# Kernel optimization log

Hardware: AMD Instinct MI355X
Metric: run time of the kernel (lower is better)

Reference implementation:

```python
import jax, jax.numpy as jnp
import numpy as np
from jax import lax

EPS = 1e-5


def setup_inputs() -> dict:
    key = jax.random.key(0)
    ks = jax.random.split(key, 4)
    B, C, H, W = 8, 256, 64, 64
    G, K = 4, 3
    x = jax.random.normal(ks[0], (B, C, H, W), dtype=jnp.float32)
    # offset/mask branch conv: 3*G*K*K output channels (2 offsets + 1 mask per point)
    w_off = jax.random.normal(ks[1], (3 * G * K * K, C, K, K), dtype=jnp.float32) * 0.01
    b_off = jnp.zeros((3 * G * K * K,), dtype=jnp.float32)
    # deformable conv weight, grouped: [C_out, C_in//G, K, K]
    w_dcn = jax.random.normal(ks[2], (C, C // G, K, K), dtype=jnp.float32) * (1.0 / np.sqrt(C // G * K * K))
    b_dcn = jnp.zeros((C,), dtype=jnp.float32)
    gamma = jnp.ones((C,), dtype=jnp.float32)
    beta = jnp.zeros((C,), dtype=jnp.float32)
    return {"x": x, "w_off": w_off, "b_off": b_off, "w_dcn": w_dcn,
            "b_dcn": b_dcn, "gamma": gamma, "beta": beta}


def _bilinear_gather(flat, idx, valid, B, G, Cg, KK, H, W):
    # flat: [B,G,Cg,H*W]; idx, valid: [B,G,KK,H,W]
    idx_f = idx.reshape(B, G, 1, KK * H * W)
    vals = jnp.take_along_axis(flat, idx_f, axis=3)  # [B,G,Cg,KK*H*W]
    vals = vals.reshape(B, G, Cg, KK, H, W)
    return vals * valid[:, :, None].astype(flat.dtype)


def _dcn_forward(x, w_off, b_off, w_dcn, b_dcn, gamma, beta):
    B, C, H, W = x.shape
    G, K = 4, 3
    KK = K * K
    Cg = C // G
    pad = K // 2
    dn = ("NCHW", "OIHW", "NCHW")

    # offset / modulation branch
    off = lax.conv_general_dilated(x, w_off, (1, 1), "SAME", dimension_numbers=dn)
    off = off + b_off[None, :, None, None]
    offsets = off[:, : 2 * G * KK].reshape(B, G, KK, 2, H, W)
    mask = jax.nn.sigmoid(off[:, 2 * G * KK:]).reshape(B, G, KK, H, W)

    # sampling locations: output pixel + kernel offset + learned offset
    ky, kx = jnp.meshgrid(jnp.arange(K) - pad, jnp.arange(K) - pad, indexing="ij")
    ky = ky.reshape(KK).astype(x.dtype)
    kx = kx.reshape(KK).astype(x.dtype)
    hh = jnp.arange(H, dtype=x.dtype)[:, None]          # [H,1]
    ww = jnp.arange(W, dtype=x.dtype)[None, :]          # [1,W]
    py = hh[None, None, None] + ky[None, None, :, None, None] + offsets[:, :, :, 0]  # [B,G,KK,H,W]
    px = ww[None, None, None] + kx[None, None, :, None, None] + offsets[:, :, :, 1]

    y0 = jnp.floor(py); x0 = jnp.floor(px)
    wy1 = py - y0; wy0 = 1.0 - wy1
    wx1 = px - x0; wx0 = 1.0 - wx1
    y0i = y0.astype(jnp.int32); x0i = x0.astype(jnp.int32)
    y1i = y0i + 1; x1i = x0i + 1

    flat = x.reshape(B, G, Cg, H * W)

    def corner(yi, xi, wgt):
        valid = (yi >= 0) & (yi < H) & (xi >= 0) & (xi < W)
        idx = jnp.clip(yi, 0, H - 1) * W + jnp.clip(xi, 0, W - 1)
        v = _bilinear_gather(flat, idx, valid, B, G, Cg, KK, H, W)
        return v * wgt[:, :, None]

    sampled = (corner(y0i, x0i, wy0 * wx0) + corner(y0i, x1i, wy0 * wx1)
               + corner(y1i, x0i, wy1 * wx0) + corner(y1i, x1i, wy1 * wx1))
    sampled = sampled * mask[:, :, None]                 # [B,G,Cg,KK,H,W]

    wg = w_dcn.reshape(G, C // G, Cg, KK)                # [G, Cout_g, Cin_g, KK]
    out = jnp.einsum("bgckhw,gock->bgohw", sampled, wg).reshape(B, C, H, W)
    out = out + b_dcn[None, :, None, None]

    # LayerNorm over channel dim (applied in BHWC layout)
    a = out.transpose(0, 2, 3, 1)                        # [B,H,W,C]
    mu = jnp.mean(a, axis=-1, keepdims=True)
    var = jnp.mean(jnp.square(a - mu), axis=-1, keepdims=True)
    normed = (a - mu) * lax.rsqrt(var + EPS) * gamma + beta
    attn = jax.nn.sigmoid(normed).transpose(0, 3, 1, 2)  # [B,C,H,W]
    return x * attn


def reference(x, w_off, b_off, w_dcn, b_dcn, gamma, beta):
    return _dcn_forward(x, w_off, b_off, w_dcn, b_dcn, gamma, beta)
```

## Files before the change

### kernel.cpp

```cpp
#include <hip/hip_runtime.h>
#include <hip/hip_bf16.h>
#include <math.h>


typedef __attribute__((ext_vector_type(4))) short s16x4;
typedef __attribute__((ext_vector_type(8))) short s16x8;
typedef __attribute__((ext_vector_type(4))) float f32x4;

union S8 { s16x8 v; s16x4 h[2]; };
union S8U { s16x8 v; unsigned u[4]; };

__device__ __forceinline__ s16x8 ld8(const short* p) {
  S8 r;
  r.h[0] = *(const s16x4*)p;
  r.h[1] = *(const s16x4*)(p + 4);
  return r.v;
}

__device__ __forceinline__ unsigned short bfr(float v) {
  unsigned u = __float_as_uint(v);
  u = (u + 0x7FFFu + ((u >> 16) & 1u)) >> 16;
  return (unsigned short)u;
}
__device__ __forceinline__ float bff(unsigned short s) {
  return __uint_as_float(((unsigned)s) << 16);
}
__device__ __forceinline__ float bf(short s) {
  return __uint_as_float(((unsigned)(unsigned short)s) << 16);
}
__device__ __forceinline__ unsigned cvtpk(float lo, float hi) {
  union { __hip_bfloat162 b; unsigned u; } cv;
  cv.b = __float22bfloat162_rn(make_float2(lo, hi));
  return cv.u;
}

__global__ __launch_bounds__(256) void k_prep(
    const float* __restrict__ w_off, const float* __restrict__ w_dcn,
    short* __restrict__ wo_a, short* __restrict__ wd_a) {
  int i = blockIdx.x * 256 + threadIdx.x;
  const int n1 = 112 * 2304;
  if (i < n1) {
    int e = i & 7;
    int t1 = i >> 3;
    int lane = t1 & 63;
    int t2 = t1 >> 6;
    int mt = t2 % 7;
    int t3 = t2 / 7;
    int s = t3 & 1;
    int t4 = t3 >> 1;
    int tap = t4 % 9;
    int part = t4 / 9;
    int co = mt * 16 + (lane & 15);
    int ch = part * 64 + s * 32 + (lane >> 4) * 8 + e;
    float v = (co < 108) ? w_off[(co * 256 + ch) * 9 + tap] : 0.f;
    wo_a[i] = (short)bfr(v);
  } else {
    int j = i - n1;
    int g = j / 36864, r = j % 36864;
    int tap = r >> 12;
    int q = r & 4095;
    int co = q >> 6, cl = q & 63;
    wd_a[j] = (short)bfr(w_dcn[((g * 64 + co) * 64 + cl) * 9 + tap]);
  }
}

__global__ __launch_bounds__(256) void k_x2(
    const float* __restrict__ x, short* __restrict__ x2) {
  int id = blockIdx.x * 256 + threadIdx.x;
  const int n1 = 8 * 32 * 4096;
  if (id < n1) {
    int pc = id & 4095;
    int c2 = (id >> 12) & 31;
    int b = id >> 17;
    int h = pc >> 6, w = pc & 63;
    const float* xp = x + ((size_t)(b * 256 + c2 * 8)) * 4096 + pc;
    short* o = x2 + ((size_t)(b * 32 + c2) * 4356 + (h + 1) * 66 + (w + 1)) * 8;
    s16x4 v0, v1;
#pragma unroll
    for (int i = 0; i < 4; ++i) {
      v0[i] = (short)bfr(xp[(size_t)i * 4096]);
      v1[i] = (short)bfr(xp[(size_t)(i + 4) * 4096]);
    }
    *(s16x4*)o = v0;
    *(s16x4*)(o + 4) = v1;
  } else {
    int j = id - n1;
    int plane = j / 260, r = j % 260;
    int h, w;
    if (r < 66) { h = 0; w = r; }
    else if (r < 132) { h = 65; w = r - 66; }
    else if (r < 196) { h = r - 131; w = 0; }
    else { h = r - 195; w = 65; }
    short* o = x2 + ((size_t)plane * 4356 + h * 66 + w) * 8;
    s16x4 z = {0, 0, 0, 0};
    *(s16x4*)o = z;
    *(s16x4*)(o + 4) = z;
  }
}

__global__ __launch_bounds__(256) void k_offconv(
    const short* __restrict__ x2, const short* __restrict__ wo_a,
    const float* __restrict__ b_off, short* __restrict__ wpart) {
  __shared__ short p_s[4 * 66 * 68];
  int bi = blockIdx.x;
  int xcd = bi & 7;
  int j = bi >> 3;
  int slice = xcd * 4 + (j & 3);
  int h0 = (j >> 2) * 2;
  int part = slice >> 3, b = slice & 7;
  int tid = threadIdx.x;
  int lane = tid & 63, wv = tid >> 6;
  int quad = lane >> 4, l15 = lane & 15;

  f32x4 zero4 = {0.f, 0.f, 0.f, 0.f};
  f32x4 acc[7][2];
#pragma unroll
  for (int i = 0; i < 7; ++i)
#pragma unroll
    for (int r = 0; r < 2; ++r) acc[i][r] = zero4;

  const short* x2b = x2 + (size_t)(b * 32 + part * 8) * 34848;
  const short* wfrag = wo_a + (size_t)part * 64512 + lane * 8;

  for (int it = tid; it < 2112; it += 256) {
    int ck = it / 264;
    int rp = it - ck * 264;
    const short* src = x2b + (size_t)ck * 34848 + ((size_t)h0 * 66 + rp) * 8;
    S8 v;
    v.v = *(const s16x8*)src;
    short* dst = &p_s[rp * 68 + ck * 8];
    *(s16x4*)dst = v.h[0];
    *(s16x4*)(dst + 4) = v.h[1];
  }
  __syncthreads();

  int nb = 16 * wv + l15;
#pragma unroll
  for (int tap = 0; tap < 9; ++tap) {
    int ky = tap / 3, kx = tap % 3;
#pragma unroll
    for (int s = 0; s < 2; ++s) {
      int k0 = 32 * s + quad * 8;
      const short* wb = wfrag + (size_t)(tap * 2 + s) * 3584;
      s16x8 af[7];
#pragma unroll
      for (int mt = 0; mt < 7; ++mt)
        af[mt] = *(const s16x8*)(wb + (size_t)mt * 512);
#pragma unroll
      for (int r = 0; r < 2; ++r) {
        s16x8 bf_f = ld8(&p_s[((r + ky) * 66 + nb + kx) * 68 + k0]);
#pragma unroll
        for (int mt = 0; mt < 7; ++mt)
          acc[mt][r] =
              __builtin_amdgcn_mfma_f32_16x16x32_bf16(af[mt], bf_f, acc[mt][r], 0, 0, 0);
      }
    }
  }

  short* wp = wpart + ((size_t)part * 8 + b) * 108 * 4096;
#pragma unroll
  for (int mt = 0; mt < 7; ++mt) {
#pragma unroll
    for (int rr = 0; rr < 2; ++rr) {
#pragma unroll
      for (int r = 0; r < 4; ++r) {
        int co = 16 * mt + quad * 4 + r;
        if (co < 108) {
          float v = acc[mt][rr][r] + (part == 0 ? b_off[co] : 0.f);
          wp[(size_t)co * 4096 + (h0 + rr) * 64 + nb] = (short)bfr(v);
        }
      }
    }
  }
}

__global__ __launch_bounds__(256) void k_dcn(
    const short* __restrict__ x2, const short* __restrict__ wpart,
    const short* __restrict__ wd_a, const float* __restrict__ b_dcn,
    float* __restrict__ dcn) {
  __shared__ float4 prm[9][64];
  __shared__ short wlds[2][64][72];

  int bi = blockIdx.x;
  int xcd = bi & 7;
  int j = bi >> 3;
  int grp = xcd * 4 + (j & 3);
  int h = j >> 2;
  int b = grp >> 2, g = grp & 3;
  int tid = threadIdx.x;
  int lane = tid & 63, wv = tid >> 6;
  int quad = lane >> 4, l15 = lane & 15;
  int px = 16 * wv + l15;

  f32x4 zero4 = {0.f, 0.f, 0.f, 0.f};
  f32x4 acc[4];
#pragma unroll
  for (int i = 0; i < 4; ++i) acc[i] = zero4;

  const short* x2g = x2 + (size_t)(b * 32 + g * 8) * 34848;
  const short* plA = x2g + (size_t)quad * 34848;
  const short* plB = x2g + (size_t)(quad + 4) * 34848;
  const short* wd_g = wd_a + (size_t)g * 36864;

  int co_w = tid >> 2, kp_w = (tid & 3) * 16;

  {
    const short* wsrc = wd_g + co_w * 64 + kp_w;
    s16x8 w0 = *(const s16x8*)wsrc;
    s16x8 w1 = *(const s16x8*)(wsrc + 8);
    *(s16x8*)&wlds[0][co_w][kp_w] = w0;
    *(s16x8*)&wlds[0][co_w][kp_w + 8] = w1;
  }
  for (int i = tid; i < 576; i += 256) {
    int c = i >> 6, pxa = i & 63;
    int sp = h * 64 + pxa;
    int co_y = (g * 9 + c) * 2;
    float oy = 0.f, ox = 0.f, mz = 0.f;
#pragma unroll
    for (int p4 = 0; p4 < 4; ++p4) {
      const short* wp = wpart + ((size_t)p4 * 8 + b) * 108 * 4096;
      oy += bff((unsigned short)wp[(size_t)co_y * 4096 + sp]);
      ox += bff((unsigned short)wp[(size_t)(co_y + 1) * 4096 + sp]);
      mz += bff((unsigned short)wp[(size_t)(72 + g * 9 + c) * 4096 + sp]);
    }
    float m = 1.f / (1.f + __expf(-mz));
    float py = (float)h + (float)(c / 3 - 1) + oy;
    float pxf = (float)pxa + (float)(c % 3 - 1) + ox;
    prm[c][pxa] = make_float4(py, pxf, m, 0.f);
  }
  __syncthreads();

  s16x8 cA[2][4], cB[2][4];
  float4 wts[2];

  auto stage = [&](int c, int st) {
    float4 pr = prm[c][px];
    float py = pr.x, pxf = pr.y, m = pr.z;
    float y0 = floorf(py), x0 = floorf(pxf);
    float wy1 = py - y0, wy0 = 1.f - wy1;
    float wx1 = pxf - x0, wx0 = 1.f - wx1;
    int y0i = (int)y0, x0i = (int)x0;
    int y1i = y0i + 1, x1i = x0i + 1;
    bool vy0 = (y0i >= 0) & (y0i < 64), vy1 = (y1i >= 0) & (y1i < 64);
    bool vx0 = (x0i >= 0) & (x0i < 64), vx1 = (x1i >= 0) & (x1i < 64);
    int cy0 = min(max(y0i, 0), 63) + 1, cy1 = min(max(y1i, 0), 63) + 1;
    int cx0 = min(max(x0i, 0), 63) + 1, cx1 = min(max(x1i, 0), 63) + 1;
    int i00 = cy0 * 66 + cx0, i01 = cy0 * 66 + cx1;
    int i10 = cy1 * 66 + cx0, i11 = cy1 * 66 + cx1;
    wts[st] = make_float4((vy0 && vx0) ? wy0 * wx0 * m : 0.f,
                          (vy0 && vx1) ? wy0 * wx1 * m : 0.f,
                          (vy1 && vx0) ? wy1 * wx0 * m : 0.f,
                          (vy1 && vx1) ? wy1 * wx1 * m : 0.f);
    cA[st][0] = *(const s16x8*)(plA + (size_t)i00 * 8);
    cA[st][1] = *(const s16x8*)(plA + (size_t)i01 * 8);
    cA[st][2] = *(const s16x8*)(plA + (size_t)i10 * 8);
    cA[st][3] = *(const s16x8*)(plA + (size_t)i11 * 8);
    cB[st][0] = *(const s16x8*)(plB + (size_t)i00 * 8);
    cB[st][1] = *(const s16x8*)(plB + (size_t)i01 * 8);
    cB[st][2] = *(const s16x8*)(plB + (size_t)i10 * 8);
    cB[st][3] = *(const s16x8*)(plB + (size_t)i11 * 8);
  };

  stage(0, 0);
#pragma unroll
  for (int c = 0; c < 9; ++c) {
    int cur = c & 1;
    s16x8 wn0, wn1;
    if (c < 8) {
      const short* wsrc = wd_g + (size_t)(c + 1) * 4096 + co_w * 64 + kp_w;
      wn0 = *(const s16x8*)wsrc;
      wn1 = *(const s16x8*)(wsrc + 8);
      stage(c + 1, cur ^ 1);
    }

    float4 w = wts[cur];
    S8U bf0, bf1;
#pragma unroll
    for (int i2 = 0; i2 < 4; ++i2) {
      int e0 = 2 * i2, e1 = 2 * i2 + 1;
      float vA0 = w.x * bf(cA[cur][0][e0]) + w.y * bf(cA[cur][1][e0]) +
                  w.z * bf(cA[cur][2][e0]) + w.w * bf(cA[cur][3][e0]);
      float vA1 = w.x * bf(cA[cur][0][e1]) + w.y * bf(cA[cur][1][e1]) +
                  w.z * bf(cA[cur][2][e1]) + w.w * bf(cA[cur][3][e1]);
      float vB0 = w.x * bf(cB[cur][0][e0]) + w.y * bf(cB[cur][1][e0]) +
                  w.z * bf(cB[cur][2][e0]) + w.w * bf(cB[cur][3][e0]);
      float vB1 = w.x * bf(cB[cur][0][e1]) + w.y * bf(cB[cur][1][e1]) +
                  w.z * bf(cB[cur][2][e1]) + w.w * bf(cB[cur][3][e1]);
      bf0.u[i2] = cvtpk(vA0, vA1);
      bf1.u[i2] = cvtpk(vB0, vB1);
    }

#pragma unroll
    for (int mt = 0; mt < 4; ++mt) {
      s16x8 af = *(const s16x8*)&wlds[cur][16 * mt + l15][quad * 8];
      acc[mt] = __builtin_amdgcn_mfma_f32_16x16x32_bf16(af, bf0.v, acc[mt], 0, 0, 0);
    }
#pragma unroll
    for (int mt = 0; mt < 4; ++mt) {
      s16x8 af = *(const s16x8*)&wlds[cur][16 * mt + l15][32 + quad * 8];
      acc[mt] = __builtin_amdgcn_mfma_f32_16x16x32_bf16(af, bf1.v, acc[mt], 0, 0, 0);
    }

    if (c < 8) {
      *(s16x8*)&wlds[cur ^ 1][co_w][kp_w] = wn0;
      *(s16x8*)&wlds[cur ^ 1][co_w][kp_w + 8] = wn1;
      __syncthreads();
    }
  }

  int nb = px;
#pragma unroll
  for (int mt = 0; mt < 4; ++mt) {
#pragma unroll
    for (int r = 0; r < 4; ++r) {
      int co = 16 * mt + quad * 4 + r;
      dcn[(((size_t)b * 256 + g * 64 + co) * 64 + h) * 64 + nb] =
          acc[mt][r] + b_dcn[g * 64 + co];
    }
  }
}

__global__ __launch_bounds__(256) void k_ln(
    const float* __restrict__ dcn, const float* __restrict__ x,
    const float* __restrict__ gamma, const float* __restrict__ beta,
    float* __restrict__ out) {
  __shared__ float red_s[4][64];
  __shared__ float red_q[4][64];
  int px = threadIdx.x & 63;
  int part = threadIdx.x >> 6;
  int p = blockIdx.x * 64 + px;
  int b = p >> 12, hw = p & 4095;
  const float* ob = dcn + (size_t)b * 256 * 4096 + hw;
  const float* xb = x + (size_t)b * 256 * 4096 + hw;
  float* yb = out + (size_t)b * 256 * 4096 + hw;
  int c0 = part * 64;
  float v[64];
  float s = 0.f, s2 = 0.f;
#pragma unroll
  for (int i = 0; i < 64; ++i) {
    v[i] = ob[(c0 + i) * 4096];
    s += v[i];
    s2 += v[i] * v[i];
  }
  red_s[part][px] = s;
  red_q[part][px] = s2;
  __syncthreads();
  s = red_s[0][px] + red_s[1][px] + red_s[2][px] + red_s[3][px];
  s2 = red_q[0][px] + red_q[1][px] + red_q[2][px] + red_q[3][px];
  float mu = s * (1.f / 256.f);
  float var = s2 * (1.f / 256.f) - mu * mu;
  float rs = rsqrtf(var + 1e-5f);
#pragma unroll
  for (int i = 0; i < 64; ++i) {
    int c = c0 + i;
    float nrm = (v[i] - mu) * rs * gamma[c] + beta[c];
    float attn = 1.f / (1.f + __expf(-nrm));
    yb[c * 4096] = xb[c * 4096] * attn;
  }
}

extern "C" void kernel_launch(void* const* d_in, const int* in_sizes, int n_in,
                              void* d_out, int out_size, void* d_ws,
                              size_t ws_size, hipStream_t stream) {
  const float* x = (const float*)d_in[0];
  const float* w_off = (const float*)d_in[1];
  const float* b_off = (const float*)d_in[2];
  const float* w_dcn = (const float*)d_in[3];
  const float* b_dcn = (const float*)d_in[4];
  const float* gamma = (const float*)d_in[5];
  const float* beta = (const float*)d_in[6];
  float* out = (float*)d_out;
  char* wsb = (char*)d_ws;

  short* wpart = (short*)wsb;
  short* wo_a = (short*)(wsb + 28311552);
  short* wd_a = (short*)(wsb + 28827648);
  short* x2 = (short*)(wsb + 29122560);
  float* dcnb = out;

  k_prep<<<1584, 256, 0, stream>>>(w_off, w_dcn, wo_a, wd_a);
  k_x2<<<4356, 256, 0, stream>>>(x, x2);
  k_offconv<<<1024, 256, 0, stream>>>(x2, wo_a, b_off, wpart);
  k_dcn<<<2048, 256, 0, stream>>>(x2, wpart, wd_a, b_dcn, dcnb);
  k_ln<<<512, 256, 0, stream>>>(dcnb, x, gamma, beta, out);
}
```

Baseline: 193.1 us.

## Repartition offset-conv MFMA tiles across waves by output-channel instead of pixel

In the offset conv kernel, each wave now owns one or two 16-channel output tiles (waves 0-2 get two, wave 3 gets one) across all 64 pixels. Previously every wave held all seven channel tiles for its own 16-pixel strip. Each wave now loads at most two weight fragments per step from global memory instead of seven, and reads four LDS B-fragments per row instead of one. This cuts redundant weight traffic and accumulator registers, but leaves the last wave with half the MFMA work, so the load across waves is uneven.

```diff
diff --git a/kernel.cpp b/kernel.cpp
--- a/kernel.cpp
+++ b/kernel.cpp
@@ -112,12 +112,17 @@
   int lane = tid & 63, wv = tid >> 6;
   int quad = lane >> 4, l15 = lane & 15;
 
+  int mt0 = 2 * wv;
+  bool two = (wv < 3);
+
   f32x4 zero4 = {0.f, 0.f, 0.f, 0.f};
-  f32x4 acc[7][2];
-#pragma unroll
-  for (int i = 0; i < 7; ++i)
-#pragma unroll
-    for (int r = 0; r < 2; ++r) acc[i][r] = zero4;
+  f32x4 acc[2][2][4];
+#pragma unroll
+  for (int a = 0; a < 2; ++a)
+#pragma unroll
+    for (int r = 0; r < 2; ++r)
+#pragma unroll
+      for (int p = 0; p < 4; ++p) acc[a][r][p] = zero4;
 
   const short* x2b = x2 + (size_t)(b * 32 + part * 8) * 34848;
   const short* wfrag = wo_a + (size_t)part * 64512 + lane * 8;
@@ -134,7 +139,6 @@
   }
   __syncthreads();
 
-  int nb = 16 * wv + l15;
 #pragma unroll
   for (int tap = 0; tap < 9; ++tap) {
     int ky = tap / 3, kx = tap % 3;
@@ -142,32 +146,41 @@
     for (int s = 0; s < 2; ++s) {
       int k0 = 32 * s + quad * 8;
       const short* wb = wfrag + (size_t)(tap * 2 + s) * 3584;
-      s16x8 af[7];
-#pragma unroll
-      for (int mt = 0; mt < 7; ++mt)
-        af[mt] = *(const s16x8*)(wb + (size_t)mt * 512);
-#pragma unroll
-      for (int r = 0; r < 2; ++r) {
-        s16x8 bf_f = ld8(&p_s[((r + ky) * 66 + nb + kx) * 68 + k0]);
-#pragma unroll
-        for (int mt = 0; mt < 7; ++mt)
-          acc[mt][r] =
-              __builtin_amdgcn_mfma_f32_16x16x32_bf16(af[mt], bf_f, acc[mt][r], 0, 0, 0);
+      s16x8 af0 = *(const s16x8*)(wb + (size_t)mt0 * 512);
+      s16x8 af1 = af0;
+      if (two) af1 = *(const s16x8*)(wb + (size_t)(mt0 + 1) * 512);
+#pragma unroll
+      for (int rr = 0; rr < 2; ++rr) {
+#pragma unroll
+        for (int pg = 0; pg < 4; ++pg) {
+          s16x8 bf_f = ld8(&p_s[((rr + ky) * 66 + pg * 16 + l15 + kx) * 68 + k0]);
+          acc[0][rr][pg] =
+              __builtin_amdgcn_mfma_f32_16x16x32_bf16(af0, bf_f, acc[0][rr][pg], 0, 0, 0);
+          if (two)
+            acc[1][rr][pg] =
+                __builtin_amdgcn_mfma_f32_16x16x32_bf16(af1, bf_f, acc[1][rr][pg], 0, 0, 0);
+        }
       }
     }
   }
 
   short* wp = wpart + ((size_t)part * 8 + b) * 108 * 4096;
 #pragma unroll
-  for (int mt = 0; mt < 7; ++mt) {
-#pragma unroll
-    for (int rr = 0; rr < 2; ++rr) {
-#pragma unroll
-      for (int r = 0; r < 4; ++r) {
-        int co = 16 * mt + quad * 4 + r;
-        if (co < 108) {
-          float v = acc[mt][rr][r] + (part == 0 ? b_off[co] : 0.f);
-          wp[(size_t)co * 4096 + (h0 + rr) * 64 + nb] = (short)bfr(v);
+  for (int ms = 0; ms < 2; ++ms) {
+    if (ms == 0 || two) {
+      int mt = mt0 + ms;
+#pragma unroll
+      for (int rr = 0; rr < 2; ++rr) {
+#pragma unroll
+        for (int pg = 0; pg < 4; ++pg) {
+#pragma unroll
+          for (int r = 0; r < 4; ++r) {
+            int co = 16 * mt + quad * 4 + r;
+            if (co < 108) {
+              float v = acc[ms][rr][pg][r] + (part == 0 ? b_off[co] : 0.f);
+              wp[(size_t)co * 4096 + (h0 + rr) * 64 + pg * 16 + l15] = (short)bfr(v);
+            }
+          }
         }
       }
     }
```

Measured after the change: 203.2 us. 1.05x slower.
